# Kernel optimization log

Measured on AMD Instinct MI355X. Metric: run time of the kernel, lower is better.

## Reference

```python
import jax, jax.numpy as jnp
import numpy as np

P = 3          # patch_length
P2 = 9         # patch_length**2
CENTER = 4     # patch_center_idx = P2 // 2
REF_LEN = 1    # reference_patch_length
EPS_SHIFT = 1e-6


def _unfold3(feat):
    # F.unfold(feat, 3, padding=1).view(B, C*9, H, W): channel order c*9 + ki*3 + kj
    B, C, H, W = feat.shape
    p = jnp.pad(feat, ((0, 0), (0, 0), (1, 1), (1, 1)))
    patches = [p[:, :, i:i + H, j:j + W] for i in range(3) for j in range(3)]
    return jnp.stack(patches, axis=2).reshape(B, C * 9, H, W)


def _mlp(x, w0, b0, w1, b1, w2, b2, w3, b3, w4, b4):
    h = jax.nn.relu(x @ w0 + b0)
    h = jax.nn.relu(h @ w1 + b1)
    h = jax.nn.relu(h @ w2 + b2)
    h = jax.nn.relu(h @ w3 + b3)
    return h @ w4 + b4


def _forward(feat, coord, cell, w0, b0, w1, b1, w2, b2, w3, b3, w4, b4):
    B, C, H, W = feat.shape
    Q = coord.shape[1]
    featu = _unfold3(feat)                      # (B, C*9, H, W)
    rx = 1.0 / H                                # 2 / H / 2
    ry = 1.0 / W
    coord_p = coord.reshape(B, Q, P2, 2)        # pairs: [...,0]=h-coord, [...,1]=w-coord
    bidx = jnp.arange(B)[:, None]
    # bug-faithful rel_coord scaling: even indices scaled by H then W, odd never
    rel_scale = jnp.array([float(H) * float(W), 1.0], coord.dtype)
    cell_scale = jnp.array([float(H), float(W)], cell.dtype)
    v_lst = [i for i in range(-REF_LEN, REF_LEN + 1) if i != 0]
    preds, areas = [], []
    for vx in v_lst:
        for vy in v_lst:
            shift = jnp.array([vx * rx + EPS_SHIFT, vy * ry + EPS_SHIFT], coord.dtype)
            center = jnp.clip(coord_p[:, :, CENTER, :] + shift, -1 + 1e-6, 1 - 1e-6)
            # nearest grid_sample, align_corners=False: idx = round((g+1)*size/2 - 0.5)
            row = jnp.clip(jnp.round((center[..., 0] + 1) * H / 2 - 0.5).astype(jnp.int32), 0, H - 1)
            col = jnp.clip(jnp.round((center[..., 1] + 1) * W / 2 - 0.5).astype(jnp.int32), 0, W - 1)
            q_feat = featu[bidx, :, row, col]                       # (B, Q, C*9)
            q_coord = jnp.stack([(2 * row + 1) / H - 1,
                                 (2 * col + 1) / W - 1], -1).astype(coord.dtype)
            rel = (coord_p - q_coord[:, :, None, :]) * rel_scale    # (B, Q, P2, 2)
            rel_flat = rel.reshape(B, Q, 2 * P2)
            rel_cell = cell * cell_scale
            x = jnp.concatenate([q_feat, rel_flat, rel_cell], axis=-1)
            pred = _mlp(x, w0, b0, w1, b1, w2, b2, w3, b3, w4, b4)  # (B, Q, 27)
            preds.append(pred)
            areas.append(jnp.abs(rel[:, :, 0, 0] * rel[:, :, 0, 1]) + 1e-9)
    tot = areas[0] + areas[1] + areas[2] + areas[3]
    # local_ensemble: swap diagonally opposite areas
    areas[0], areas[3] = areas[3], areas[0]
    areas[1], areas[2] = areas[2], areas[1]
    ret = jnp.zeros_like(preds[0])
    for p_, a_ in zip(preds, areas):
        ret = ret + p_ * (a_ / tot)[..., None]
    return ret


def setup_inputs() -> dict:
    key = jax.random.key(0)
    ks = jax.random.split(key, 8)
    B, C, H, W, Q = 8, 64, 48, 48, 8192
    HID, OUT = 256, 27
    in_dim = C * 9 + 2 * P2 + 2  # 596
    feat = jax.random.normal(ks[0], (B, C, H, W), jnp.float32)
    coord = jax.random.uniform(ks[1], (B, Q, 2 * P2), jnp.float32, -1.0, 1.0)
    cell = jnp.full((B, Q, 2), 2.0 / (H * 4), jnp.float32)

    def lin(k, fi, fo):
        return (jax.random.normal(k, (fi, fo), jnp.float32) / np.sqrt(fi)).astype(jnp.float32)

    return {
        'feat': feat, 'coord': coord, 'cell': cell,
        'w0': lin(ks[2], in_dim, HID), 'b0': jnp.zeros((HID,), jnp.float32),
        'w1': lin(ks[3], HID, HID), 'b1': jnp.zeros((HID,), jnp.float32),
        'w2': lin(ks[4], HID, HID), 'b2': jnp.zeros((HID,), jnp.float32),
        'w3': lin(ks[5], HID, HID), 'b3': jnp.zeros((HID,), jnp.float32),
        'w4': lin(ks[6], HID, OUT), 'b4': jnp.zeros((OUT,), jnp.float32),
    }


def reference(feat, coord, cell, w0, b0, w1, b1, w2, b2, w3, b3, w4, b4):
    return _forward(feat, coord, cell, w0, b0, w1, b1, w2, b2, w3, b3, w4, b4)
```

## Files before the change

kernel.cpp:

```cpp
#include <hip/hip_runtime.h>
#include <hip/hip_bf16.h>

typedef _Float16 f16x8 __attribute__((ext_vector_type(8)));
typedef float f32x4 __attribute__((ext_vector_type(4)));

#define BQ 65536
#define KPAD0 640
#define HID 256
#define NOUT 27
#define ZOFF 1179648

#define WAITVM(n) __builtin_amdgcn_s_waitcnt(0x0F70 | (n))

__device__ __forceinline__ void gl_lds16(const _Float16* g, _Float16* l) {
    __builtin_amdgcn_global_load_lds(
        (const __attribute__((address_space(1))) void*)g,
        (__attribute__((address_space(3))) void*)l, 16, 0, 0);
}

__global__ __launch_bounds__(256) void feat_transpose(
    const float* __restrict__ feat, _Float16* __restrict__ featT,
    _Float16* __restrict__ zbuf)
{
    __shared__ float tile[64 * 49];
    int bh = blockIdx.x;
    int b = bh / 48, h = bh - b * 48;
    int t = threadIdx.x;
    if (bh == 0 && t < 128) zbuf[t] = (_Float16)0.f;
    #pragma unroll
    for (int i = 0; i < 12; i++) {
        int idx = t + i * 256;
        int c = idx / 48, w = idx - c * 48;
        tile[c * 49 + w] = feat[(((size_t)b * 64 + c) * 48 + h) * 48 + w];
    }
    __syncthreads();
    #pragma unroll
    for (int i = 0; i < 12; i++) {
        int idx = t + i * 256;
        int w = idx >> 6, c = idx & 63;
        featT[(((size_t)b * 48 + h) * 48 + w) * 64 + c] = (_Float16)tile[c * 49 + w];
    }
}

__global__ void transpose_cast(const float* __restrict__ w, _Float16* __restrict__ wt,
                               int Kin, int Nin, int Kpad, int Npad) {
    int idx = blockIdx.x * 256 + threadIdx.x;
    if (idx >= Npad * Kpad) return;
    int n = idx / Kpad, k = idx - n * Kpad;
    float v = (n < Nin && k < Kin) ? w[k * Nin + n] : 0.f;
    wt[idx] = (_Float16)v;
}

__global__ void transpose_cast_w0(const float* __restrict__ w0, _Float16* __restrict__ wt) {
    int idx = blockIdx.x * 256 + threadIdx.x;
    if (idx >= 256 * KPAD0) return;
    int n = idx / KPAD0, kp = idx - n * KPAD0;
    int src = (kp < 576) ? ((kp & 63) * 9 + (kp >> 6)) : kp;
    float v = (src < 596) ? w0[src * 256 + n] : 0.f;
    wt[idx] = (_Float16)v;
}

__global__ __launch_bounds__(256, 2) void mega(
    const _Float16* __restrict__ featT, const float* __restrict__ coord,
    const float* __restrict__ cell,
    const _Float16* __restrict__ W0t, const _Float16* __restrict__ W1t,
    const _Float16* __restrict__ W2t, const _Float16* __restrict__ W3t,
    const _Float16* __restrict__ W4t,
    const float* __restrict__ b0, const float* __restrict__ b1,
    const float* __restrict__ b2, const float* __restrict__ b3,
    const float* __restrict__ b4, float* __restrict__ preds)
{
    __shared__ _Float16 act[64 * 256];
    __shared__ _Float16 Bsw[4][2][2048];
    __shared__ int   rc_s[64][2];
    __shared__ float q_s[64][2];
    __shared__ float wgt[64];

    int t = threadIdx.x;
    int wave = t >> 6, lane = t & 63;
    int lrow = lane & 15, lq = lane >> 4;
    int blk = blockIdx.x;
    int s = blk & 3;
    int bq0 = (blk >> 2) * 64;

    if (t < 64) {
        int bq = bq0 + t;
        const float* cp = coord + (size_t)bq * 18;
        float areas[4]; int mri = 0, mci = 0; float mqx = 0.f, mqy = 0.f;
        #pragma unroll
        for (int ss = 0; ss < 4; ss++) {
            float vx = (ss & 2) ? 1.f : -1.f, vy = (ss & 1) ? 1.f : -1.f;
            float cx = cp[8] + vx * (1.f / 48.f) + 1e-6f;
            float cy = cp[9] + vy * (1.f / 48.f) + 1e-6f;
            cx = fminf(fmaxf(cx, -1.f + 1e-6f), 1.f - 1e-6f);
            cy = fminf(fmaxf(cy, -1.f + 1e-6f), 1.f - 1e-6f);
            int ri = (int)rintf((cx + 1.f) * 24.f - 0.5f); ri = min(max(ri, 0), 47);
            int ci = (int)rintf((cy + 1.f) * 24.f - 0.5f); ci = min(max(ci, 0), 47);
            float qx = (float)(2 * ri + 1) / 48.f - 1.f;
            float qy = (float)(2 * ci + 1) / 48.f - 1.f;
            areas[ss] = fabsf((cp[0] - qx) * 2304.f * (cp[1] - qy)) + 1e-9f;
            if (ss == s) { mri = ri; mci = ci; mqx = qx; mqy = qy; }
        }
        float tot = areas[0] + areas[1] + areas[2] + areas[3];
        wgt[t] = areas[s ^ 3] / tot;
        rc_s[t][0] = mri; rc_s[t][1] = mci;
        q_s[t][0] = mqx;  q_s[t][1] = mqy;
    }
    __syncthreads();

    int gdat = (lane & 3) ^ ((lane >> 3) & 3);
    int rsl  = lane >> 2;

    int rA[4], cA[4], bA[4];
    #pragma unroll
    for (int j = 0; j < 4; j++) {
        int arow = j * 16 + rsl;
        rA[j] = rc_s[arow][0];
        cA[j] = rc_s[arow][1];
        bA[j] = ((bq0 + arow) >> 13) * 147456;
    }

    f32x4 acc[4][4];
    #pragma unroll
    for (int mi = 0; mi < 4; mi++)
        #pragma unroll
        for (int ni = 0; ni < 4; ni++) acc[mi][ni] = (f32x4){0.f, 0.f, 0.f, 0.f};

    {
        auto stageL0 = [&](int step, int buf) {
            int p = step >> 1, half = step & 1;
            int di = p / 3 - 1, dj = p - (p / 3) * 3 - 1;
            int k0 = p * 64 + half * 32;
            #pragma unroll
            for (int j = 0; j < 4; j++) {
                int r2 = rA[j] + di, c2 = cA[j] + dj;
                int off = ((unsigned)r2 < 48u && (unsigned)c2 < 48u)
                        ? bA[j] + ((r2 * 48 + c2) << 6) : ZOFF;
                gl_lds16(featT + off + half * 32 + gdat * 8,
                         act + wave * 4096 + buf * 2048 + j * 512);
                gl_lds16(W0t + (size_t)(wave * 64 + j * 16 + rsl) * KPAD0 + k0 + gdat * 8,
                         &Bsw[wave][buf][j * 512]);
            }
        };
        stageL0(0, 0);
        #pragma unroll
        for (int step = 0; step < 18; step++) {
            if (step < 17) { stageL0(step + 1, (step + 1) & 1); WAITVM(8); }
            else           { WAITVM(0); }
            const _Float16* Ab = act + wave * 4096 + (step & 1) * 2048;
            const _Float16* Bb = &Bsw[wave][step & 1][0];
            f16x8 af[4], bf[4];
            #pragma unroll
            for (int mi = 0; mi < 4; mi++) {
                int row = mi * 16 + lrow;
                af[mi] = *(const f16x8*)&Ab[row * 32 + ((lq ^ ((row >> 1) & 3)) << 3)];
            }
            #pragma unroll
            for (int ni = 0; ni < 4; ni++) {
                int row = ni * 16 + lrow;
                bf[ni] = *(const f16x8*)&Bb[row * 32 + ((lq ^ ((row >> 1) & 3)) << 3)];
            }
            #pragma unroll
            for (int mi = 0; mi < 4; mi++)
                #pragma unroll
                for (int ni = 0; ni < 4; ni++)
                    acc[mi][ni] = __builtin_amdgcn_mfma_f32_16x16x32_f16(
                        af[mi], bf[ni], acc[mi][ni], 0, 0, 0);
        }
    }
    {
        f16x8 af[4], bf[4];
        #pragma unroll
        for (int mi = 0; mi < 4; mi++) {
            int row = mi * 16 + lrow;
            int bq = bq0 + row;
            const float* cp2 = coord + (size_t)bq * 18;
            float qx = q_s[row][0], qy = q_s[row][1];
            _Float16 tmp[8];
            #pragma unroll
            for (int j = 0; j < 8; j++) {
                int idx = lq * 8 + j;
                float v;
                if (idx < 18) v = (idx & 1) ? (cp2[idx] - qy) : ((cp2[idx] - qx) * 2304.f);
                else if (idx == 18) v = cell[(size_t)bq * 2] * 48.f;
                else if (idx == 19) v = cell[(size_t)bq * 2 + 1] * 48.f;
                else v = 0.f;
                tmp[j] = (_Float16)v;
            }
            af[mi] = *(f16x8*)tmp;
        }
        #pragma unroll
        for (int ni = 0; ni < 4; ni++) {
            int br = wave * 64 + ni * 16 + lrow;
            bf[ni] = *(const f16x8*)&W0t[(size_t)br * KPAD0 + 576 + lq * 8];
        }
        #pragma unroll
        for (int mi = 0; mi < 4; mi++)
            #pragma unroll
            for (int ni = 0; ni < 4; ni++)
                acc[mi][ni] = __builtin_amdgcn_mfma_f32_16x16x32_f16(
                    af[mi], bf[ni], acc[mi][ni], 0, 0, 0);
    }
    __syncthreads();
    {
        float bvv[4];
        #pragma unroll
        for (int ni = 0; ni < 4; ni++) bvv[ni] = b0[wave * 64 + ni * 16 + lrow];
        #pragma unroll
        for (int mi = 0; mi < 4; mi++)
            #pragma unroll
            for (int ni = 0; ni < 4; ni++) {
                int cw = wave * 64 + ni * 16 + lrow;
                #pragma unroll
                for (int rr = 0; rr < 4; rr++) {
                    float v = acc[mi][ni][rr] + bvv[ni];
                    v = v > 0.f ? v : 0.f;
                    int rw = mi * 16 + lq * 4 + rr;
                    int gp = ((cw >> 3) ^ (rw & 31)) & 31;
                    act[rw * 256 + gp * 8 + (cw & 7)] = (_Float16)v;
                }
            }
    }
    __syncthreads();

    for (int layer = 0; layer < 3; layer++) {
        const _Float16* Wl = (layer == 0) ? W1t : (layer == 1) ? W2t : W3t;
        const float*    bl = (layer == 0) ? b1  : (layer == 1) ? b2  : b3;
        auto stageH = [&](int k, int buf) {
            #pragma unroll
            for (int j = 0; j < 4; j++)
                gl_lds16(Wl + (size_t)(wave * 64 + j * 16 + rsl) * 256 + k * 32 + gdat * 8,
                         &Bsw[wave][buf][j * 512]);
        };
        #pragma unroll
        for (int mi = 0; mi < 4; mi++)
            #pragma unroll
            for (int ni = 0; ni < 4; ni++) acc[mi][ni] = (f32x4){0.f, 0.f, 0.f, 0.f};
        stageH(0, 0);
        #pragma unroll
        for (int k = 0; k < 8; k++) {
            if (k < 7) { stageH(k + 1, (k + 1) & 1); WAITVM(4); }
            else       { WAITVM(0); }
            const _Float16* Bb = &Bsw[wave][k & 1][0];
            f16x8 af[4], bf[4];
            #pragma unroll
            for (int mi = 0; mi < 4; mi++) {
                int ar = mi * 16 + lrow;
                int gp = (((k * 4) + lq) ^ (ar & 31)) & 31;
                af[mi] = *(const f16x8*)&act[ar * 256 + gp * 8];
            }
            #pragma unroll
            for (int ni = 0; ni < 4; ni++) {
                int row = ni * 16 + lrow;
                bf[ni] = *(const f16x8*)&Bb[row * 32 + ((lq ^ ((row >> 1) & 3)) << 3)];
            }
            #pragma unroll
            for (int mi = 0; mi < 4; mi++)
                #pragma unroll
                for (int ni = 0; ni < 4; ni++)
                    acc[mi][ni] = __builtin_amdgcn_mfma_f32_16x16x32_f16(
                        af[mi], bf[ni], acc[mi][ni], 0, 0, 0);
        }
        __syncthreads();
        {
            float bvv[4];
            #pragma unroll
            for (int ni = 0; ni < 4; ni++) bvv[ni] = bl[wave * 64 + ni * 16 + lrow];
            #pragma unroll
            for (int mi = 0; mi < 4; mi++)
                #pragma unroll
                for (int ni = 0; ni < 4; ni++) {
                    int cw = wave * 64 + ni * 16 + lrow;
                    #pragma unroll
                    for (int rr = 0; rr < 4; rr++) {
                        float v = acc[mi][ni][rr] + bvv[ni];
                        v = v > 0.f ? v : 0.f;
                        int rw = mi * 16 + lq * 4 + rr;
                        int gp = ((cw >> 3) ^ (rw & 31)) & 31;
                        act[rw * 256 + gp * 8 + (cw & 7)] = (_Float16)v;
                    }
                }
        }
        __syncthreads();
    }

    f32x4 acc2[2];
    acc2[0] = (f32x4){0.f, 0.f, 0.f, 0.f};
    acc2[1] = (f32x4){0.f, 0.f, 0.f, 0.f};
    int mrow0 = wave * 16;
    {
        auto stage4 = [&](int k, int buf) {
            #pragma unroll
            for (int j = 0; j < 2; j++)
                gl_lds16(W4t + (size_t)(j * 16 + rsl) * 256 + k * 32 + gdat * 8,
                         &Bsw[wave][buf][j * 512]);
        };
        stage4(0, 0);
        #pragma unroll
        for (int k = 0; k < 8; k++) {
            if (k < 7) { stage4(k + 1, (k + 1) & 1); WAITVM(2); }
            else       { WAITVM(0); }
            const _Float16* Bb = &Bsw[wave][k & 1][0];
            f16x8 af, bf[2];
            {
                int ar = mrow0 + lrow;
                int gp = (((k * 4) + lq) ^ (ar & 31)) & 31;
                af = *(const f16x8*)&act[ar * 256 + gp * 8];
            }
            #pragma unroll
            for (int ni = 0; ni < 2; ni++) {
                int row = ni * 16 + lrow;
                bf[ni] = *(const f16x8*)&Bb[row * 32 + ((lq ^ ((row >> 1) & 3)) << 3)];
            }
            #pragma unroll
            for (int ni = 0; ni < 2; ni++)
                acc2[ni] = __builtin_amdgcn_mfma_f32_16x16x32_f16(af, bf[ni], acc2[ni], 0, 0, 0);
        }
    }

    {
        float bv0 = b4[lrow];
        float bv1 = (lrow < 11) ? b4[16 + lrow] : 0.f;
        float* pr = preds + (size_t)s * (BQ * NOUT);
        #pragma unroll
        for (int rr = 0; rr < 4; rr++) {
            int row = mrow0 + lq * 4 + rr;
            float w = wgt[row];
            size_t obase = (size_t)(bq0 + row) * 27;
            pr[obase + lrow] = w * (acc2[0][rr] + bv0);
            if (lrow < 11)
                pr[obase + 16 + lrow] = w * (acc2[1][rr] + bv1);
        }
    }
}

__global__ __launch_bounds__(256) void combine_kernel(
    const float* __restrict__ preds, float* __restrict__ out)
{
    int idx = blockIdx.x * 256 + threadIdx.x;
    if (idx >= BQ * NOUT) return;
    const size_t st = (size_t)BQ * NOUT;
    out[idx] = preds[idx] + preds[st + idx] + preds[2 * st + idx] + preds[3 * st + idx];
}

extern "C" void kernel_launch(void* const* d_in, const int* in_sizes, int n_in,
                              void* d_out, int out_size, void* d_ws, size_t ws_size,
                              hipStream_t stream) {
    const float* feat  = (const float*)d_in[0];
    const float* coord = (const float*)d_in[1];
    const float* cell  = (const float*)d_in[2];
    const float* w0 = (const float*)d_in[3];  const float* b0 = (const float*)d_in[4];
    const float* w1 = (const float*)d_in[5];  const float* b1 = (const float*)d_in[6];
    const float* w2 = (const float*)d_in[7];  const float* b2 = (const float*)d_in[8];
    const float* w3 = (const float*)d_in[9];  const float* b3 = (const float*)d_in[10];
    const float* w4 = (const float*)d_in[11]; const float* b4 = (const float*)d_in[12];
    float* out = (float*)d_out;

    char* ws = (char*)d_ws;
    size_t off = 0;
    _Float16* W0t = (_Float16*)(ws + off); off += (size_t)256 * KPAD0 * 2;
    _Float16* W1t = (_Float16*)(ws + off); off += (size_t)256 * 256 * 2;
    _Float16* W2t = (_Float16*)(ws + off); off += (size_t)256 * 256 * 2;
    _Float16* W3t = (_Float16*)(ws + off); off += (size_t)256 * 256 * 2;
    _Float16* W4t = (_Float16*)(ws + off); off += (size_t)32 * 256 * 2;
    _Float16* featT = (_Float16*)(ws + off); off += (size_t)ZOFF * 2;
    _Float16* zbuf  = (_Float16*)(ws + off); off += 512;
    float* preds    = (float*)(ws + off);    off += (size_t)4 * BQ * NOUT * 4;

    feat_transpose<<<8 * 48, 256, 0, stream>>>(feat, featT, zbuf);
    transpose_cast_w0<<<(256 * KPAD0 + 255) / 256, 256, 0, stream>>>(w0, W0t);
    transpose_cast<<<256, 256, 0, stream>>>(w1, W1t, 256, 256, 256, 256);
    transpose_cast<<<256, 256, 0, stream>>>(w2, W2t, 256, 256, 256, 256);
    transpose_cast<<<256, 256, 0, stream>>>(w3, W3t, 256, 256, 256, 256);
    transpose_cast<<<32, 256, 0, stream>>>(w4, W4t, 256, NOUT, 256, 32);

    mega<<<4 * (BQ / 64), 256, 0, stream>>>(featT, coord, cell,
                                            W0t, W1t, W2t, W3t, W4t,
                                            b0, b1, b2, b3, b4, preds);

    combine_kernel<<<(BQ * NOUT + 255) / 256, 256, 0, stream>>>(preds, out);
}
```

Baseline: 365.4 us.

## Merge prep kernels into one launch and single-buffer LDS weight staging

The six preprocessing launches (feature transpose plus five weight transpose-casts) become one prep kernel that dispatches on block index, removing launch overhead. In the main fused MLP kernel the double-buffered LDS staging for weights and L0 activations is cut to a single buffer. Each step now waits for all loads, runs its MFMAs, and only then issues the next stage's loads behind a sched_barrier. This shrinks LDS per block, which may allow more resident blocks, but it gives up load/compute overlap within a wave and relies on other waves to hide latency.

Result: slower. 458.9 us (+25.6%).

```diff
diff --git a/kernel.cpp b/kernel.cpp
--- a/kernel.cpp
+++ b/kernel.cpp
@@ -18,46 +18,59 @@
         (__attribute__((address_space(3))) void*)l, 16, 0, 0);
 }
 
-__global__ __launch_bounds__(256) void feat_transpose(
-    const float* __restrict__ feat, _Float16* __restrict__ featT,
-    _Float16* __restrict__ zbuf)
+__global__ __launch_bounds__(256) void prep(
+    const float* __restrict__ feat, const float* __restrict__ w0,
+    const float* __restrict__ w1, const float* __restrict__ w2,
+    const float* __restrict__ w3, const float* __restrict__ w4,
+    _Float16* __restrict__ featT, _Float16* __restrict__ zbuf,
+    _Float16* __restrict__ W0t, _Float16* __restrict__ W1t,
+    _Float16* __restrict__ W2t, _Float16* __restrict__ W3t,
+    _Float16* __restrict__ W4t)
 {
     __shared__ float tile[64 * 49];
-    int bh = blockIdx.x;
-    int b = bh / 48, h = bh - b * 48;
-    int t = threadIdx.x;
-    if (bh == 0 && t < 128) zbuf[t] = (_Float16)0.f;
-    #pragma unroll
-    for (int i = 0; i < 12; i++) {
-        int idx = t + i * 256;
-        int c = idx / 48, w = idx - c * 48;
-        tile[c * 49 + w] = feat[(((size_t)b * 64 + c) * 48 + h) * 48 + w];
-    }
-    __syncthreads();
-    #pragma unroll
-    for (int i = 0; i < 12; i++) {
-        int idx = t + i * 256;
-        int w = idx >> 6, c = idx & 63;
-        featT[(((size_t)b * 48 + h) * 48 + w) * 64 + c] = (_Float16)tile[c * 49 + w];
-    }
-}
-
-__global__ void transpose_cast(const float* __restrict__ w, _Float16* __restrict__ wt,
-                               int Kin, int Nin, int Kpad, int Npad) {
-    int idx = blockIdx.x * 256 + threadIdx.x;
-    if (idx >= Npad * Kpad) return;
-    int n = idx / Kpad, k = idx - n * Kpad;
-    float v = (n < Nin && k < Kin) ? w[k * Nin + n] : 0.f;
-    wt[idx] = (_Float16)v;
-}
-
-__global__ void transpose_cast_w0(const float* __restrict__ w0, _Float16* __restrict__ wt) {
-    int idx = blockIdx.x * 256 + threadIdx.x;
-    if (idx >= 256 * KPAD0) return;
-    int n = idx / KPAD0, kp = idx - n * KPAD0;
-    int src = (kp < 576) ? ((kp & 63) * 9 + (kp >> 6)) : kp;
-    float v = (src < 596) ? w0[src * 256 + n] : 0.f;
-    wt[idx] = (_Float16)v;
+    int bid = blockIdx.x, t = threadIdx.x;
+    if (bid < 384) {
+        int b = bid / 48, h = bid - b * 48;
+        if (bid == 0 && t < 128) zbuf[t] = (_Float16)0.f;
+        #pragma unroll
+        for (int i = 0; i < 12; i++) {
+            int idx = t + i * 256;
+            int c = idx / 48, w = idx - c * 48;
+            tile[c * 49 + w] = feat[(((size_t)b * 64 + c) * 48 + h) * 48 + w];
+        }
+        __syncthreads();
+        #pragma unroll
+        for (int i = 0; i < 12; i++) {
+            int idx = t + i * 256;
+            int w = idx >> 6, c = idx & 63;
+            featT[(((size_t)b * 48 + h) * 48 + w) * 64 + c] = (_Float16)tile[c * 49 + w];
+        }
+        return;
+    }
+    int r = bid - 384;
+    if (r < 640) {
+        int idx = r * 256 + t;
+        int n = idx / KPAD0, kp = idx - n * KPAD0;
+        int src = (kp < 576) ? ((kp & 63) * 9 + (kp >> 6)) : kp;
+        W0t[idx] = (_Float16)((src < 596) ? w0[src * 256 + n] : 0.f);
+        return;
+    }
+    r -= 640;
+    if (r < 768) {
+        int which = r >> 8;
+        int idx = (r & 255) * 256 + t;
+        int n = idx >> 8, k = idx & 255;
+        const float* w = (which == 0) ? w1 : (which == 1) ? w2 : w3;
+        _Float16* wt  = (which == 0) ? W1t : (which == 1) ? W2t : W3t;
+        wt[idx] = (_Float16)w[k * 256 + n];
+        return;
+    }
+    r -= 768;
+    {
+        int idx = r * 256 + t;
+        int n = idx >> 8, k = idx & 255;
+        W4t[idx] = (_Float16)((n < NOUT) ? w4[k * NOUT + n] : 0.f);
+    }
 }
 
 __global__ __launch_bounds__(256, 2) void mega(
@@ -71,7 +84,7 @@
     const float* __restrict__ b4, float* __restrict__ preds)
 {
     __shared__ _Float16 act[64 * 256];
-    __shared__ _Float16 Bsw[4][2][2048];
+    __shared__ _Float16 Bsw[4][2048];
     __shared__ int   rc_s[64][2];
     __shared__ float q_s[64][2];
     __shared__ float wgt[64];
@@ -127,28 +140,27 @@
         for (int ni = 0; ni < 4; ni++) acc[mi][ni] = (f32x4){0.f, 0.f, 0.f, 0.f};
 
     {
-        auto stageL0 = [&](int step, int buf) {
-            int p = step >> 1, half = step & 1;
+        auto stageL0 = [&](int st) {
+            int p = st >> 1, half = st & 1;
             int di = p / 3 - 1, dj = p - (p / 3) * 3 - 1;
-            int k0 = p * 64 + half * 32;
             #pragma unroll
             for (int j = 0; j < 4; j++) {
                 int r2 = rA[j] + di, c2 = cA[j] + dj;
                 int off = ((unsigned)r2 < 48u && (unsigned)c2 < 48u)
                         ? bA[j] + ((r2 * 48 + c2) << 6) : ZOFF;
                 gl_lds16(featT + off + half * 32 + gdat * 8,
-                         act + wave * 4096 + buf * 2048 + j * 512);
-                gl_lds16(W0t + (size_t)(wave * 64 + j * 16 + rsl) * KPAD0 + k0 + gdat * 8,
-                         &Bsw[wave][buf][j * 512]);
+                         act + wave * 2048 + j * 512);
+                gl_lds16(W0t + (size_t)(wave * 64 + j * 16 + rsl) * KPAD0
+                             + p * 64 + half * 32 + gdat * 8,
+                         &Bsw[wave][j * 512]);
             }
         };
-        stageL0(0, 0);
-        #pragma unroll
-        for (int step = 0; step < 18; step++) {
-            if (step < 17) { stageL0(step + 1, (step + 1) & 1); WAITVM(8); }
-            else           { WAITVM(0); }
-            const _Float16* Ab = act + wave * 4096 + (step & 1) * 2048;
-            const _Float16* Bb = &Bsw[wave][step & 1][0];
+        stageL0(0);
+        #pragma unroll
+        for (int st = 0; st < 18; st++) {
+            WAITVM(0);
+            const _Float16* Ab = act + wave * 2048;
+            const _Float16* Bb = &Bsw[wave][0];
             f16x8 af[4], bf[4];
             #pragma unroll
             for (int mi = 0; mi < 4; mi++) {
@@ -166,6 +178,8 @@
                 for (int ni = 0; ni < 4; ni++)
                     acc[mi][ni] = __builtin_amdgcn_mfma_f32_16x16x32_f16(
                         af[mi], bf[ni], acc[mi][ni], 0, 0, 0);
+            __builtin_amdgcn_sched_barrier(0);
+            if (st < 17) stageL0(st + 1);
         }
     }
     {
@@ -226,22 +240,21 @@
     for (int layer = 0; layer < 3; layer++) {
         const _Float16* Wl = (layer == 0) ? W1t : (layer == 1) ? W2t : W3t;
         const float*    bl = (layer == 0) ? b1  : (layer == 1) ? b2  : b3;
-        auto stageH = [&](int k, int buf) {
+        auto stageH = [&](int k) {
             #pragma unroll
             for (int j = 0; j < 4; j++)
                 gl_lds16(Wl + (size_t)(wave * 64 + j * 16 + rsl) * 256 + k * 32 + gdat * 8,
-                         &Bsw[wave][buf][j * 512]);
+                         &Bsw[wave][j * 512]);
         };
         #pragma unroll
         for (int mi = 0; mi < 4; mi++)
             #pragma unroll
             for (int ni = 0; ni < 4; ni++) acc[mi][ni] = (f32x4){0.f, 0.f, 0.f, 0.f};
-        stageH(0, 0);
+        stageH(0);
         #pragma unroll
         for (int k = 0; k < 8; k++) {
-            if (k < 7) { stageH(k + 1, (k + 1) & 1); WAITVM(4); }
-            else       { WAITVM(0); }
-            const _Float16* Bb = &Bsw[wave][k & 1][0];
+            WAITVM(0);
+            const _Float16* Bb = &Bsw[wave][0];
             f16x8 af[4], bf[4];
             #pragma unroll
             for (int mi = 0; mi < 4; mi++) {
@@ -260,6 +273,8 @@
                 for (int ni = 0; ni < 4; ni++)
                     acc[mi][ni] = __builtin_amdgcn_mfma_f32_16x16x32_f16(
                         af[mi], bf[ni], acc[mi][ni], 0, 0, 0);
+            __builtin_amdgcn_sched_barrier(0);
+            if (k < 7) stageH(k + 1);
         }
         __syncthreads();
         {
@@ -289,18 +304,17 @@
     acc2[1] = (f32x4){0.f, 0.f, 0.f, 0.f};
     int mrow0 = wave * 16;
     {
-        auto stage4 = [&](int k, int buf) {
+        auto stage4 = [&](int k) {
             #pragma unroll
             for (int j = 0; j < 2; j++)
                 gl_lds16(W4t + (size_t)(j * 16 + rsl) * 256 + k * 32 + gdat * 8,
-                         &Bsw[wave][buf][j * 512]);
+                         &Bsw[wave][j * 512]);
         };
-        stage4(0, 0);
+        stage4(0);
         #pragma unroll
         for (int k = 0; k < 8; k++) {
-            if (k < 7) { stage4(k + 1, (k + 1) & 1); WAITVM(2); }
-            else       { WAITVM(0); }
-            const _Float16* Bb = &Bsw[wave][k & 1][0];
+            WAITVM(0);
+            const _Float16* Bb = &Bsw[wave][0];
             f16x8 af, bf[2];
             {
                 int ar = mrow0 + lrow;
@@ -309,12 +323,14 @@
             }
             #pragma unroll
             for (int ni = 0; ni < 2; ni++) {
-                int row = ni * 16 + lrow;
-                bf[ni] = *(const f16x8*)&Bb[row * 32 + ((lq ^ ((row >> 1) & 3)) << 3)];
+                int r2 = ni * 16 + lrow;
+                bf[ni] = *(const f16x8*)&Bb[r2 * 32 + ((lq ^ ((r2 >> 1) & 3)) << 3)];
             }
             #pragma unroll
             for (int ni = 0; ni < 2; ni++)
                 acc2[ni] = __builtin_amdgcn_mfma_f32_16x16x32_f16(af, bf[ni], acc2[ni], 0, 0, 0);
+            __builtin_amdgcn_sched_barrier(0);
+            if (k < 7) stage4(k + 1);
         }
     }
 
@@ -364,15 +380,11 @@
     _Float16* W3t = (_Float16*)(ws + off); off += (size_t)256 * 256 * 2;
     _Float16* W4t = (_Float16*)(ws + off); off += (size_t)32 * 256 * 2;
     _Float16* featT = (_Float16*)(ws + off); off += (size_t)ZOFF * 2;
-    _Float16* zbuf  = (_Float16*)(ws + off); off += 512;
+    _Float16* zbuf  = (_Float16*)(ws + off); off += 1024;
     float* preds    = (float*)(ws + off);    off += (size_t)4 * BQ * NOUT * 4;
 
-    feat_transpose<<<8 * 48, 256, 0, stream>>>(feat, featT, zbuf);
-    transpose_cast_w0<<<(256 * KPAD0 + 255) / 256, 256, 0, stream>>>(w0, W0t);
-    transpose_cast<<<256, 256, 0, stream>>>(w1, W1t, 256, 256, 256, 256);
-    transpose_cast<<<256, 256, 0, stream>>>(w2, W2t, 256, 256, 256, 256);
-    transpose_cast<<<256, 256, 0, stream>>>(w3, W3t, 256, 256, 256, 256);
-    transpose_cast<<<32, 256, 0, stream>>>(w4, W4t, 256, NOUT, 256, 32);
+    prep<<<1824, 256, 0, stream>>>(feat, w0, w1, w2, w3, w4,
+                                   featT, zbuf, W0t, W1t, W2t, W3t, W4t);
 
     mega<<<4 * (BQ / 64), 256, 0, stream>>>(featT, coord, cell,
                                             W0t, W1t, W2t, W3t, W4t,
```
